# Performance work log

Measured on AMD Instinct MI355X. Metric: run time of the kernel, lower is better.

The kernel has to match this reference:

```python
import jax, jax.numpy as jnp
import numpy as np

K_STEPS = 10
ALPHA = 0.1


def setup_inputs() -> dict:
    key = jax.random.key(0)
    k0, k1, k2, k3 = jax.random.split(key, 4)
    N, E, C_IN, C_HID, C_OUT = 100000, 3200000, 512, 256, 64
    x = jax.random.normal(k0, (N, C_IN), dtype=jnp.float32)
    edge_index = jax.random.randint(k1, (2, E), 0, N, dtype=jnp.int64)
    W1 = jax.random.normal(k2, (C_IN, C_HID), dtype=jnp.float32) * (1.0 / np.sqrt(C_IN))
    b1 = jnp.zeros((C_HID,), dtype=jnp.float32)
    W2 = jax.random.normal(k3, (C_HID, C_OUT), dtype=jnp.float32) * (1.0 / np.sqrt(C_HID))
    b2 = jnp.zeros((C_OUT,), dtype=jnp.float32)
    return {"x": x, "edge_index": edge_index, "W1": W1, "b1": b1, "W2": W2, "b2": b2}


def reference(x, edge_index, W1, b1, W2, b2):
    N = x.shape[0]
    src, dst = edge_index[0], edge_index[1]
    # add self-loops (PyG APPNP default)
    loop = jnp.arange(N, dtype=src.dtype)
    src = jnp.concatenate([src, loop])
    dst = jnp.concatenate([dst, loop])
    # GCN symmetric normalization: D^{-1/2} A D^{-1/2}
    deg = jax.ops.segment_sum(jnp.ones_like(dst, dtype=x.dtype), dst, num_segments=N)
    dinv = jnp.where(deg > 0, deg ** -0.5, jnp.zeros_like(deg))
    norm = dinv[src] * dinv[dst]  # [E+N]
    # MLP (dropout is identity at inference)
    h = jax.nn.relu(x @ W1 + b1) @ W2 + b2  # [N, C_OUT]
    # K-step APPNP propagation with teleport
    out = h
    for _ in range(K_STEPS):
        msg = norm[:, None] * out[src]  # [E+N, C_OUT]
        agg = jax.ops.segment_sum(msg, dst, num_segments=N)
        out = (1.0 - ALPHA) * agg + ALPHA * h
    return jax.nn.log_softmax(out, axis=1)
```

## Files before the change

kernel.cpp:

```cpp
#include <hip/hip_runtime.h>
#include <hip/hip_bf16.h>

#define C_IN  512
#define C_HID 256
#define C_OUT 64
#define K_STEPS 10
#define ALPHA 0.1f

#define BKT_SHIFT 9
#define BKT_NODES 512
#define BCAP 24576
#define EPB 4096

typedef _Float16 half8 __attribute__((ext_vector_type(8)));
typedef float f32x4 __attribute__((ext_vector_type(4)));


__global__ __launch_bounds__(256) void k_bucketA(
    const int* __restrict__ src, const int* __restrict__ dst, int E,
    int* __restrict__ bcursor, long long* __restrict__ bedges, int nbkt)
{
    __shared__ int lcount[256];
    __shared__ int lbase[256];
    int t = threadIdx.x;
    int base = blockIdx.x * EPB;
    for (int i = t; i < nbkt; i += 256) lcount[i] = 0;
    __syncthreads();

    int       mybkt[16];
    int       myoff[16];
    long long mypk[16];
    #pragma unroll
    for (int j = 0; j < 16; j++) {
        int e = base + j * 256 + t;
        if (e < E) {
            int s = src[e], d = dst[e];
            int b = d >> BKT_SHIFT;
            mybkt[j] = b;
            mypk[j]  = ((long long)d << 32) | (unsigned int)s;
            myoff[j] = atomicAdd(&lcount[b], 1);
        } else {
            mybkt[j] = -1;
        }
    }
    __syncthreads();
    for (int i = t; i < nbkt; i += 256)
        lbase[i] = lcount[i] ? atomicAdd(&bcursor[i], lcount[i]) : 0;
    __syncthreads();
    #pragma unroll
    for (int j = 0; j < 16; j++) {
        if (mybkt[j] >= 0) {
            int p = lbase[mybkt[j]] + myoff[j];
            bedges[(size_t)mybkt[j] * BCAP + p] = mypk[j];
        }
    }
}

__global__ __launch_bounds__(256) void k_bcount(
    const int* __restrict__ bcursor, const long long* __restrict__ bedges,
    int* __restrict__ counts, int N)
{
    __shared__ int lcnt[BKT_NODES];
    int b = blockIdx.x, t = threadIdx.x;
    int nodebase = b << BKT_SHIFT;
    for (int i = t; i < BKT_NODES; i += 256) lcnt[i] = 0;
    __syncthreads();
    int cnt = bcursor[b];
    const long long* be = bedges + (size_t)b * BCAP;
    for (int i = t; i < cnt; i += 256) {
        int d = (int)(be[i] >> 32);
        atomicAdd(&lcnt[d - nodebase], 1);
    }
    __syncthreads();
    for (int i = t; i < BKT_NODES; i += 256) {
        int node = nodebase + i;
        if (node < N) counts[node] = lcnt[i];
    }
}

__global__ __launch_bounds__(256) void k_bscatter(
    const int* __restrict__ bcursor, const long long* __restrict__ bedges,
    const int* __restrict__ rowptr, int* __restrict__ csr_src, int N)
{
    __shared__ int lcur[BKT_NODES];
    int b = blockIdx.x, t = threadIdx.x;
    int nodebase = b << BKT_SHIFT;
    for (int i = t; i < BKT_NODES; i += 256) {
        int node = nodebase + i;
        lcur[i] = (node < N) ? rowptr[node] : 0;
    }
    __syncthreads();
    int cnt = bcursor[b];
    const long long* be = bedges + (size_t)b * BCAP;
    for (int i = t; i < cnt; i += 256) {
        long long pk = be[i];
        int d = (int)(pk >> 32);
        int s = (int)pk;
        int p = atomicAdd(&lcur[d - nodebase], 1);
        csr_src[p] = s;
    }
}


__global__ void k_dinv(const int* __restrict__ counts, float* __restrict__ dinv, int N) {
    int i = blockIdx.x * blockDim.x + threadIdx.x;
    if (i < N) {
        float deg = (float)(counts[i] + 1);
        dinv[i] = 1.0f / sqrtf(deg);
    }
}

#define SCAN_CHUNK 2048

__global__ void k_scan1(const int* __restrict__ counts, int N, int* __restrict__ bsum) {
    __shared__ int sdata[256];
    int b = blockIdx.x, t = threadIdx.x;
    int base = b * SCAN_CHUNK;
    int sum = 0;
    for (int i = t; i < SCAN_CHUNK; i += 256) {
        int idx = base + i;
        sum += (idx < N) ? counts[idx] : 0;
    }
    sdata[t] = sum;
    __syncthreads();
    for (int off = 128; off; off >>= 1) {
        if (t < off) sdata[t] += sdata[t + off];
        __syncthreads();
    }
    if (t == 0) bsum[b] = sdata[0];
}

__global__ void k_scan2(int* __restrict__ bsum, int nb, int E, int* __restrict__ rowptr, int N) {
    if (blockIdx.x == 0 && threadIdx.x == 0) {
        int run = 0;
        for (int i = 0; i < nb; i++) { int v = bsum[i]; bsum[i] = run; run += v; }
        rowptr[N] = E;
    }
}

__global__ void k_scan3(const int* __restrict__ counts, int N,
                        const int* __restrict__ bsum, int* __restrict__ rowptr) {
    __shared__ int sdata[256];
    int b = blockIdx.x, t = threadIdx.x;
    int base = b * SCAN_CHUNK;
    int vals[8];
    int local = 0;
    #pragma unroll
    for (int i = 0; i < 8; i++) {
        int idx = base + t * 8 + i;
        vals[i] = (idx < N) ? counts[idx] : 0;
        local += vals[i];
    }
    sdata[t] = local;
    __syncthreads();
    for (int off = 1; off < 256; off <<= 1) {
        int y = 0;
        if (t >= off) y = sdata[t - off];
        __syncthreads();
        sdata[t] += y;
        __syncthreads();
    }
    int excl = (t == 0) ? 0 : sdata[t - 1];
    int run = bsum[b] + excl;
    #pragma unroll
    for (int i = 0; i < 8; i++) {
        int idx = base + t * 8 + i;
        if (idx < N) rowptr[idx] = run;
        run += vals[i];
    }
}


__global__ void k_w1t(const float* __restrict__ W, _Float16* __restrict__ Wt) {
    int i = blockIdx.x * 256 + threadIdx.x;
    int k = i >> 8, n = i & 255;
    Wt[(size_t)n * 512 + k] = (_Float16)W[i];
}

__global__ void k_w2t(const float* __restrict__ W, _Float16* __restrict__ Wt) {
    int i = blockIdx.x * 256 + threadIdx.x;
    int k = i >> 6, n = i & 63;
    Wt[(size_t)n * 256 + k] = (_Float16)W[i];
}


__global__ __launch_bounds__(128, 2) void k_mlp1(
    const float* __restrict__ A, const _Float16* __restrict__ Bt,
    const float* __restrict__ bias, _Float16* __restrict__ C, int M)
{
    extern __shared__ __align__(16) _Float16 atile[];

    int t    = threadIdx.x;
    int lane = t & 63;
    int wc   = t >> 6;
    int bm   = blockIdx.x * 64;
    int mrow = lane & 15;
    int kg   = lane >> 4;

    #pragma unroll
    for (int j = 0; j < 32; j++) {
        int chunk = j * 128 + t;
        int r = chunk >> 6;
        int c = chunk & 63;
        int gr = bm + r;
        if (gr >= M) gr = M - 1;
        const float* p = A + (size_t)gr * 512 + c * 8;
        float4 lo = *(const float4*)p;
        float4 hi = *(const float4*)(p + 4);
        half8 v;
        v[0] = (_Float16)lo.x; v[1] = (_Float16)lo.y;
        v[2] = (_Float16)lo.z; v[3] = (_Float16)lo.w;
        v[4] = (_Float16)hi.x; v[5] = (_Float16)hi.y;
        v[6] = (_Float16)hi.z; v[7] = (_Float16)hi.w;
        int cs = c ^ (r & 7);
        *(half8*)&atile[(size_t)r * 512 + cs * 8] = v;
    }
    __syncthreads();

    f32x4 acc[4][8] = {};
    for (int ks = 0; ks < 16; ks++) {
        half8 b[8];
        #pragma unroll
        for (int ni = 0; ni < 8; ni++) {
            int n = wc * 128 + ni * 16 + mrow;
            b[ni] = *(const half8*)(Bt + (size_t)n * 512 + ks * 32 + kg * 8);
        }
        half8 a[4];
        #pragma unroll
        for (int mi = 0; mi < 4; mi++) {
            int r = mi * 16 + mrow;
            int c = ks * 4 + kg;
            a[mi] = *(const half8*)&atile[(size_t)r * 512 + (c ^ (r & 7)) * 8];
        }
        #pragma unroll
        for (int mi = 0; mi < 4; mi++)
            #pragma unroll
            for (int ni = 0; ni < 8; ni++)
                acc[mi][ni] = __builtin_amdgcn_mfma_f32_16x16x32_f16(
                    a[mi], b[ni], acc[mi][ni], 0, 0, 0);
    }

    #pragma unroll
    for (int mi = 0; mi < 4; mi++) {
        #pragma unroll
        for (int ni = 0; ni < 8; ni++) {
            int n = wc * 128 + ni * 16 + mrow;
            float bv = bias[n];
            #pragma unroll
            for (int rg = 0; rg < 4; rg++) {
                int row = bm + mi * 16 + kg * 4 + rg;
                if (row < M) {
                    float v = acc[mi][ni][rg] + bv;
                    C[(size_t)row * 256 + n] = (_Float16)fmaxf(v, 0.f);
                }
            }
        }
    }
}


__global__ __launch_bounds__(256) void k_mlp2(
    const _Float16* __restrict__ A, const _Float16* __restrict__ Bt,
    const float* __restrict__ bias, const float* __restrict__ dinv,
    _Float16* __restrict__ C, _Float16* __restrict__ Y, int M)
{
    int lane = threadIdx.x & 63;
    int wid  = threadIdx.x >> 6;
    int bm   = blockIdx.x * 256 + wid * 64;
    int mrow = lane & 15;
    int kg   = lane >> 4;
    f32x4 acc[4][4] = {};

    int r[4];
    #pragma unroll
    for (int mi = 0; mi < 4; mi++) {
        int rr = bm + mi * 16 + mrow;
        r[mi] = rr < M ? rr : M - 1;
    }

    for (int k0 = 0; k0 < 256; k0 += 32) {
        int k = k0 + kg * 8;
        half8 a[4], b[4];
        #pragma unroll
        for (int mi = 0; mi < 4; mi++)
            a[mi] = *(const half8*)(A + (size_t)r[mi] * 256 + k);
        #pragma unroll
        for (int ni = 0; ni < 4; ni++) {
            int n = ni * 16 + mrow;
            b[ni] = *(const half8*)(Bt + (size_t)n * 256 + k);
        }
        #pragma unroll
        for (int mi = 0; mi < 4; mi++)
            #pragma unroll
            for (int ni = 0; ni < 4; ni++)
                acc[mi][ni] = __builtin_amdgcn_mfma_f32_16x16x32_f16(
                    a[mi], b[ni], acc[mi][ni], 0, 0, 0);
    }

    #pragma unroll
    for (int mi = 0; mi < 4; mi++) {
        #pragma unroll
        for (int ni = 0; ni < 4; ni++) {
            int n = ni * 16 + mrow;
            float bv = bias[n];
            #pragma unroll
            for (int rg = 0; rg < 4; rg++) {
                int row = bm + mi * 16 + kg * 4 + rg;
                if (row < M) {
                    float v = acc[mi][ni][rg] + bv;
                    C[(size_t)row * 64 + n] = (_Float16)v;
                    Y[(size_t)row * 64 + n] = (_Float16)(v * dinv[row]);
                }
            }
        }
    }
}


template <bool LAST>
__global__ __launch_bounds__(256) void k_prop(
    const int* __restrict__ rowptr, const int* __restrict__ csr_src,
    const float* __restrict__ dinv, const _Float16* __restrict__ h,
    const _Float16* __restrict__ ycur, _Float16* __restrict__ ynxt,
    float* __restrict__ out, int N)
{
    int node = blockIdx.x * 4 + (threadIdx.x >> 6);
    if (node >= N) return;
    int lane = threadIdx.x & 63;
    int g  = lane >> 3;
    int cg = lane & 7;

    int beg = rowptr[node], end = rowptr[node + 1];
    float dn = dinv[node];
    half8 ys = *(const half8*)(ycur + ((size_t)node << 6) + cg * 8);
    half8 hv = *(const half8*)(h    + ((size_t)node << 6) + cg * 8);

    float acc[8] = {};
    for (int e = beg + g; e < end; e += 32) {
        int i1 = e + 8, i2 = e + 16, i3 = e + 24;
        float p1 = (i1 < end) ? 1.f : 0.f;
        float p2 = (i2 < end) ? 1.f : 0.f;
        float p3 = (i3 < end) ? 1.f : 0.f;
        int s0 = csr_src[e];
        int s1 = csr_src[(i1 < end) ? i1 : e];
        int s2 = csr_src[(i2 < end) ? i2 : e];
        int s3 = csr_src[(i3 < end) ? i3 : e];
        half8 v0 = *(const half8*)(ycur + ((size_t)s0 << 6) + cg * 8);
        half8 v1 = *(const half8*)(ycur + ((size_t)s1 << 6) + cg * 8);
        half8 v2 = *(const half8*)(ycur + ((size_t)s2 << 6) + cg * 8);
        half8 v3 = *(const half8*)(ycur + ((size_t)s3 << 6) + cg * 8);
        #pragma unroll
        for (int c = 0; c < 8; c++)
            acc[c] += ((float)v0[c] + p1 * (float)v1[c])
                    + (p2 * (float)v2[c] + p3 * (float)v3[c]);
    }

    #pragma unroll
    for (int c = 0; c < 8; c++) {
        float a = acc[c];
        a += __shfl_xor(a, 8);
        a += __shfl_xor(a, 16);
        a += __shfl_xor(a, 32);
        acc[c] = a;
    }

    float o[8];
    #pragma unroll
    for (int c = 0; c < 8; c++)
        o[c] = (1.0f - ALPHA) * dn * (acc[c] + (float)ys[c]) + ALPHA * (float)hv[c];

    if (!LAST) {
        if (g == 0) {
            half8 w;
            #pragma unroll
            for (int c = 0; c < 8; c++) w[c] = (_Float16)(dn * o[c]);
            *(half8*)(ynxt + ((size_t)node << 6) + cg * 8) = w;
        }
    } else {
        float m = o[0];
        #pragma unroll
        for (int c = 1; c < 8; c++) m = fmaxf(m, o[c]);
        m = fmaxf(m, __shfl_xor(m, 1));
        m = fmaxf(m, __shfl_xor(m, 2));
        m = fmaxf(m, __shfl_xor(m, 4));
        float s = 0.f;
        #pragma unroll
        for (int c = 0; c < 8; c++) s += __expf(o[c] - m);
        s += __shfl_xor(s, 1);
        s += __shfl_xor(s, 2);
        s += __shfl_xor(s, 4);
        float ls = m + logf(s);
        if (g == 0) {
            f32x4 w0, w1;
            #pragma unroll
            for (int c = 0; c < 4; c++) { w0[c] = o[c] - ls; w1[c] = o[c + 4] - ls; }
            float* p = out + ((size_t)node << 6) + cg * 8;
            *(f32x4*)p = w0;
            *(f32x4*)(p + 4) = w1;
        }
    }
}


extern "C" void kernel_launch(void* const* d_in, const int* in_sizes, int n_in,
                              void* d_out, int out_size, void* d_ws, size_t ws_size,
                              hipStream_t stream) {
    const float* x  = (const float*)d_in[0];
    const int*   ei = (const int*)d_in[1];
    const float* W1 = (const float*)d_in[2];
    const float* b1 = (const float*)d_in[3];
    const float* W2 = (const float*)d_in[4];
    const float* b2 = (const float*)d_in[5];

    const int N = in_sizes[0] / C_IN;
    const int E = in_sizes[1] / 2;
    const int* src = ei;
    const int* dst = ei + E;

    char* ws = (char*)d_ws;
    size_t off = 0;
    auto alloc = [&](size_t bytes) -> void* {
        void* p = ws + off;
        off += (bytes + 255) & ~(size_t)255;
        return p;
    };

    int nb   = (N + SCAN_CHUNK - 1) / SCAN_CHUNK;
    int nbkt = (N + BKT_NODES - 1) / BKT_NODES;

    int*       counts  = (int*)      alloc((size_t)4 * N);
    int*       rowptr  = (int*)      alloc((size_t)4 * (N + 1));
    float*     dinv    = (float*)    alloc((size_t)4 * N);
    int*       bsum    = (int*)      alloc((size_t)4 * (nb + 1));
    int*       bcursor = (int*)      alloc((size_t)4 * nbkt);
    int*       csr_src = (int*)      alloc((size_t)4 * E);
    _Float16*  W1t     = (_Float16*) alloc((size_t)2 * C_IN * C_HID);
    _Float16*  W2t     = (_Float16*) alloc((size_t)2 * C_HID * C_OUT);
    _Float16*  hmid    = (_Float16*) alloc((size_t)2 * N * C_HID);
    _Float16*  h       = (_Float16*) alloc((size_t)2 * N * C_OUT);
    _Float16*  ybuf0   = (_Float16*) alloc((size_t)2 * N * C_OUT);
    _Float16*  ybuf1   = (_Float16*) alloc((size_t)2 * N * C_OUT);
    _Float16*  ybuf2   = (_Float16*) alloc((size_t)2 * N * C_OUT);

    long long* bedges = (long long*)hmid;

    hipMemsetAsync(bcursor, 0, (size_t)4 * nbkt, stream);
    k_bucketA<<<(E + EPB - 1) / EPB, 256, 0, stream>>>(src, dst, E, bcursor, bedges, nbkt);
    k_bcount<<<nbkt, 256, 0, stream>>>(bcursor, bedges, counts, N);
    k_dinv<<<(N + 255) / 256, 256, 0, stream>>>(counts, dinv, N);
    k_scan1<<<nb, 256, 0, stream>>>(counts, N, bsum);
    k_scan2<<<1, 64, 0, stream>>>(bsum, nb, E, rowptr, N);
    k_scan3<<<nb, 256, 0, stream>>>(counts, N, bsum, rowptr);
    k_bscatter<<<nbkt, 256, 0, stream>>>(bcursor, bedges, rowptr, csr_src, N);

    k_w1t<<<(C_IN * C_HID) / 256, 256, 0, stream>>>(W1, W1t);
    k_w2t<<<(C_HID * C_OUT) / 256, 256, 0, stream>>>(W2, W2t);
    k_mlp1<<<(N + 63) / 64, 128, 65536, stream>>>(x, W1t, b1, hmid, N);
    k_mlp2<<<(N + 255) / 256, 256, 0, stream>>>(hmid, W2t, b2, dinv, h, ybuf0, N);

    int pgrid = (N + 3) / 4;
    _Float16* ycur = ybuf0;
    for (int it = 0; it < K_STEPS - 1; ++it) {
        _Float16* ynxt = (it & 1) ? ybuf2 : ybuf1;
        k_prop<false><<<pgrid, 256, 0, stream>>>(rowptr, csr_src, dinv, h, ycur, ynxt, nullptr, N);
        ycur = ynxt;
    }
    k_prop<true><<<pgrid, 256, 0, stream>>>(rowptr, csr_src, dinv, h, ycur, nullptr, (float*)d_out, N);
}
```

Baseline: 797.2 us.

## Double-buffer MLP1 A tiles via async global-to-LDS loads with smaller row tiles

Restructures the first MLP GEMM so each block handles 32 rows with 4 waves instead of 64 rows with 2 waves. The A tile is no longer loaded into 64KB of LDS in one pass. K-slices of fp32 input are streamed into a small double-buffered LDS area with global_load_lds and converted to fp16 at fragment-read time. This is meant to overlap the x loads with MFMA work and cut LDS use to raise occupancy. In exchange it adds a barrier per K step and makes each block re-read W1t for fewer rows.

```diff
diff --git a/kernel.cpp b/kernel.cpp
--- a/kernel.cpp
+++ b/kernel.cpp
@@ -184,67 +184,90 @@
 }
 
 
-__global__ __launch_bounds__(128, 2) void k_mlp1(
+__global__ __launch_bounds__(256, 4) void k_mlp1(
     const float* __restrict__ A, const _Float16* __restrict__ Bt,
     const float* __restrict__ bias, _Float16* __restrict__ C, int M)
 {
-    extern __shared__ __align__(16) _Float16 atile[];
+    __shared__ float lds[2][32 * 32];
 
     int t    = threadIdx.x;
     int lane = t & 63;
-    int wc   = t >> 6;
-    int bm   = blockIdx.x * 64;
+    int wid  = t >> 6;
+    int bm   = blockIdx.x * 32;
     int mrow = lane & 15;
     int kg   = lane >> 4;
 
-    #pragma unroll
-    for (int j = 0; j < 32; j++) {
-        int chunk = j * 128 + t;
-        int r = chunk >> 6;
-        int c = chunk & 63;
-        int gr = bm + r;
+    {
+    }
+    int sr = t >> 3;
+    int sc = (t & 7) ^ (sr & 7);
+    const float* gsrc;
+    {
+        int gr = bm + sr;
         if (gr >= M) gr = M - 1;
-        const float* p = A + (size_t)gr * 512 + c * 8;
-        float4 lo = *(const float4*)p;
-        float4 hi = *(const float4*)(p + 4);
-        half8 v;
-        v[0] = (_Float16)lo.x; v[1] = (_Float16)lo.y;
-        v[2] = (_Float16)lo.z; v[3] = (_Float16)lo.w;
-        v[4] = (_Float16)hi.x; v[5] = (_Float16)hi.y;
-        v[6] = (_Float16)hi.z; v[7] = (_Float16)hi.w;
-        int cs = c ^ (r & 7);
-        *(half8*)&atile[(size_t)r * 512 + cs * 8] = v;
-    }
-    __syncthreads();
-
-    f32x4 acc[4][8] = {};
+        gsrc = A + (size_t)gr * 512 + sc * 4;
+    }
+
+    #define STAGE(buf, ks)                                                       \
+        __builtin_amdgcn_global_load_lds(                                        \
+            (const __attribute__((address_space(1))) void*)(gsrc + (ks) * 32),   \
+            (__attribute__((address_space(3))) void*)((char*)&lds[buf][0] + t * 16), \
+            16, 0, 0);
+
+    f32x4 acc[2][4] = {};
+
+    int rbase[2], p0[2], p1[2];
+    #pragma unroll
+    for (int mi = 0; mi < 2; mi++) {
+        int r = mi * 16 + mrow;
+        rbase[mi] = r * 32;
+        p0[mi] = ((2 * kg) ^ (r & 7)) * 4;
+        p1[mi] = ((2 * kg + 1) ^ (r & 7)) * 4;
+    }
+
+    STAGE(0, 0);
+    __syncthreads();
+
+    int cur = 0;
+    #pragma unroll
     for (int ks = 0; ks < 16; ks++) {
-        half8 b[8];
-        #pragma unroll
-        for (int ni = 0; ni < 8; ni++) {
-            int n = wc * 128 + ni * 16 + mrow;
+        if (ks < 15) STAGE(cur ^ 1, ks + 1);
+
+        half8 b[4];
+        #pragma unroll
+        for (int ni = 0; ni < 4; ni++) {
+            int n = wid * 64 + ni * 16 + mrow;
             b[ni] = *(const half8*)(Bt + (size_t)n * 512 + ks * 32 + kg * 8);
         }
-        half8 a[4];
-        #pragma unroll
-        for (int mi = 0; mi < 4; mi++) {
-            int r = mi * 16 + mrow;
-            int c = ks * 4 + kg;
-            a[mi] = *(const half8*)&atile[(size_t)r * 512 + (c ^ (r & 7)) * 8];
-        }
-        #pragma unroll
-        for (int mi = 0; mi < 4; mi++)
-            #pragma unroll
-            for (int ni = 0; ni < 8; ni++)
+
+        half8 a[2];
+        #pragma unroll
+        for (int mi = 0; mi < 2; mi++) {
+            f32x4 lo = *(const f32x4*)&lds[cur][rbase[mi] + p0[mi]];
+            f32x4 hi = *(const f32x4*)&lds[cur][rbase[mi] + p1[mi]];
+            a[mi][0] = (_Float16)lo[0]; a[mi][1] = (_Float16)lo[1];
+            a[mi][2] = (_Float16)lo[2]; a[mi][3] = (_Float16)lo[3];
+            a[mi][4] = (_Float16)hi[0]; a[mi][5] = (_Float16)hi[1];
+            a[mi][6] = (_Float16)hi[2]; a[mi][7] = (_Float16)hi[3];
+        }
+
+        #pragma unroll
+        for (int mi = 0; mi < 2; mi++)
+            #pragma unroll
+            for (int ni = 0; ni < 4; ni++)
                 acc[mi][ni] = __builtin_amdgcn_mfma_f32_16x16x32_f16(
                     a[mi], b[ni], acc[mi][ni], 0, 0, 0);
-    }
-
-    #pragma unroll
-    for (int mi = 0; mi < 4; mi++) {
-        #pragma unroll
-        for (int ni = 0; ni < 8; ni++) {
-            int n = wc * 128 + ni * 16 + mrow;
+
+        __syncthreads();
+        cur ^= 1;
+    }
+    #undef STAGE
+
+    #pragma unroll
+    for (int mi = 0; mi < 2; mi++) {
+        #pragma unroll
+        for (int ni = 0; ni < 4; ni++) {
+            int n = wid * 64 + ni * 16 + mrow;
             float bv = bias[n];
             #pragma unroll
             for (int rg = 0; rg < 4; rg++) {
@@ -455,7 +478,7 @@
 
     k_w1t<<<(C_IN * C_HID) / 256, 256, 0, stream>>>(W1, W1t);
     k_w2t<<<(C_HID * C_OUT) / 256, 256, 0, stream>>>(W2, W2t);
-    k_mlp1<<<(N + 63) / 64, 128, 65536, stream>>>(x, W1t, b1, hmid, N);
+    k_mlp1<<<(N + 31) / 32, 256, 0, stream>>>(x, W1t, b1, hmid, N);
     k_mlp2<<<(N + 255) / 256, 256, 0, stream>>>(hmid, W2t, b2, dinv, h, ybuf0, N);
 
     int pgrid = (N + 3) / 4;
```

After: 808.9 us. About the same (+1.5%).
